# Performance work log

Hardware: AMD Instinct MI355X
Metric: run time of the kernel (lower is better)

## Reference

```python
import jax, jax.numpy as jnp
import numpy as np

N_SRC0, N_DST0, N_DST1 = 100000, 20000, 4000
E0, E1 = 640000, 128000
IN_F, HID_F, OUT_F = 512, 512, 256


def _graph_conv(x_src, src, dst, W, b, n_src, n_dst):
    """DGL GraphConv, norm='both': D_out^{-1/2} A D_in^{-1/2} X W + b."""
    ones_e = jnp.ones(src.shape[0], x_src.dtype)
    out_deg = jnp.maximum(jax.ops.segment_sum(ones_e, src, num_segments=n_src), 1.0)
    in_deg = jnp.maximum(jax.ops.segment_sum(ones_e, dst, num_segments=n_dst), 1.0)
    h = x_src * (out_deg ** -0.5)[:, None]          # [n_src, F] pre-normalize
    agg = jax.ops.segment_sum(h[src], dst, num_segments=n_dst)  # gather -> scatter-add
    agg = agg * (in_deg ** -0.5)[:, None]           # [n_dst, F]
    return agg @ W + b


def setup_inputs() -> dict:
    key = jax.random.key(0)
    ks = jax.random.split(key, 8)
    x = jax.random.normal(ks[0], (N_SRC0, IN_F), jnp.float32)
    src0 = jax.random.randint(ks[1], (E0,), 0, N_SRC0)
    dst0 = jax.random.randint(ks[2], (E0,), 0, N_DST0)
    src1 = jax.random.randint(ks[3], (E1,), 0, N_DST0)
    dst1 = jax.random.randint(ks[4], (E1,), 0, N_DST1)
    W1 = jax.random.normal(ks[5], (IN_F, HID_F), jnp.float32) * (IN_F ** -0.5)
    b1 = jnp.zeros((HID_F,), jnp.float32)
    W2 = jax.random.normal(ks[6], (HID_F, OUT_F), jnp.float32) * (HID_F ** -0.5)
    b2 = jnp.zeros((OUT_F,), jnp.float32)
    return {"x": x, "src0": src0, "dst0": dst0, "src1": src1, "dst1": dst1,
            "W1": W1, "b1": b1, "W2": W2, "b2": b2,
            "n_src0": N_SRC0, "n_dst0": N_DST0, "n_dst1": N_DST1}


def reference(x, src0, dst0, src1, dst1, W1, b1, W2, b2, n_src0, n_dst0, n_dst1):
    h = jax.nn.relu(_graph_conv(x, src0, dst0, W1, b1, n_src0, n_dst0))
    out = jax.nn.relu(_graph_conv(h, src1, dst1, W2, b2, n_dst0, n_dst1))
    return out
```

## Files before the change

kernel.cpp:

```cpp
#include <hip/hip_runtime.h>

typedef unsigned short ushort_t;
typedef unsigned int uint_t;
typedef __attribute__((ext_vector_type(8))) short s8v;
typedef __attribute__((ext_vector_type(4))) float f4v;

#define NS0 100000
#define ND0 20000
#define ND1 4000
#define E0  640000
#define E1  128000
#define F   512
#define OF  256
#define NCNT (NS0 + ND0 + ND0 + ND1)
#define SB  96

#define WBLK ((F * F + F * OF) / 256)

__device__ __forceinline__ ushort_t f2b(float f) {
    uint_t u = __float_as_uint(f);
    uint_t r = (u + 0x7fffu + ((u >> 16) & 1u)) >> 16;
    return (ushort_t)r;
}
__device__ __forceinline__ float b2f_lo(uint_t u) { return __uint_as_float(u << 16); }
__device__ __forceinline__ float b2f_hi(uint_t u) { return __uint_as_float(u & 0xffff0000u); }

__global__ __launch_bounds__(256) void prep(const int* __restrict__ src0, const int* __restrict__ dst0,
                                            const int* __restrict__ src1, const int* __restrict__ dst1,
                                            int* __restrict__ cntOut0, int* __restrict__ cntIn0,
                                            int* __restrict__ cntOut1, int* __restrict__ cntIn1,
                                            int* __restrict__ es0, int* __restrict__ es1,
                                            const float* __restrict__ W1, const float* __restrict__ W2,
                                            ushort_t* __restrict__ wt1, ushort_t* __restrict__ wt2) {
    int b = blockIdx.x;
    if (b < 625) {
        int e = (b * 256 + threadIdx.x) * 4;
        int4 s = *(const int4*)(src0 + e);
        int4 d = *(const int4*)(dst0 + e);
        atomicAdd(&cntOut0[s.x], 1);
        atomicAdd(&cntOut0[s.y], 1);
        atomicAdd(&cntOut0[s.z], 1);
        atomicAdd(&cntOut0[s.w], 1);
        int p0 = atomicAdd(&cntIn0[d.x], 1);
        int p1 = atomicAdd(&cntIn0[d.y], 1);
        int p2 = atomicAdd(&cntIn0[d.z], 1);
        int p3 = atomicAdd(&cntIn0[d.w], 1);
        es0[d.x * SB + min(p0, SB - 1)] = s.x;
        es0[d.y * SB + min(p1, SB - 1)] = s.y;
        es0[d.z * SB + min(p2, SB - 1)] = s.z;
        es0[d.w * SB + min(p3, SB - 1)] = s.w;
        return;
    }
    if (b < 750) {
        int e = ((b - 625) * 256 + threadIdx.x) * 4;
        int4 s = *(const int4*)(src1 + e);
        int4 d = *(const int4*)(dst1 + e);
        atomicAdd(&cntOut1[s.x], 1);
        atomicAdd(&cntOut1[s.y], 1);
        atomicAdd(&cntOut1[s.z], 1);
        atomicAdd(&cntOut1[s.w], 1);
        int p0 = atomicAdd(&cntIn1[d.x], 1);
        int p1 = atomicAdd(&cntIn1[d.y], 1);
        int p2 = atomicAdd(&cntIn1[d.z], 1);
        int p3 = atomicAdd(&cntIn1[d.w], 1);
        es1[d.x * SB + min(p0, SB - 1)] = s.x;
        es1[d.y * SB + min(p1, SB - 1)] = s.y;
        es1[d.z * SB + min(p2, SB - 1)] = s.z;
        es1[d.w * SB + min(p3, SB - 1)] = s.w;
        return;
    }
    int i = (b - 750) * 256 + threadIdx.x;
    if (i < F * F) {
        int k = i >> 9, n = i & (F - 1);
        wt1[n * F + k] = f2b(W1[i]);
    } else {
        int j = i - F * F;
        int k = j >> 8, n = j & (OF - 1);
        wt2[n * F + k] = f2b(W2[j]);
    }
}

__device__ __forceinline__ void add8(float* acc, uint4 u) {
    acc[0] += b2f_lo(u.x); acc[1] += b2f_hi(u.x);
    acc[2] += b2f_lo(u.y); acc[3] += b2f_hi(u.y);
    acc[4] += b2f_lo(u.z); acc[5] += b2f_hi(u.z);
    acc[6] += b2f_lo(u.w); acc[7] += b2f_hi(u.w);
}

__global__ __launch_bounds__(256) void agg_l1(const float* __restrict__ X, const int* __restrict__ es,
                                              const int* __restrict__ cntIn, const int* __restrict__ cntOut,
                                              ushort_t* __restrict__ out, int ndst) {
    int d = __builtin_amdgcn_readfirstlane(blockIdx.x * 4 + (threadIdx.x >> 6));
    if (d >= ndst) return;
    int lane = threadIdx.x & 63;
    int n = min(cntIn[d], SB);
    const int* ed = es + (size_t)d * SB;
    const f4v* Xv = (const f4v*)X;
    f4v accA = {0.f, 0.f, 0.f, 0.f};
    f4v accB = {0.f, 0.f, 0.f, 0.f};
    int c = n >> 2;
    int i = c << 2;
    if (c > 0) {
        int idP[4], idQ[4];
        f4v aP[4], bP[4], aQ[4], bQ[4];
        int cvP[4], cvQ[4];
        #pragma unroll
        for (int j = 0; j < 4; ++j) idP[j] = ed[j];
        #pragma unroll
        for (int j = 0; j < 4; ++j) {
            aP[j] = Xv[(size_t)idP[j] * 128 + lane];
            bP[j] = Xv[(size_t)idP[j] * 128 + 64 + lane];
        }
        #pragma unroll
        for (int j = 0; j < 4; ++j) cvP[j] = cntOut[idP[j]];
        if (c > 1) {
            #pragma unroll
            for (int j = 0; j < 4; ++j) idQ[j] = ed[4 + j];
        }
        int k = 0;
        while (true) {
            if (k + 1 < c) {
                #pragma unroll
                for (int j = 0; j < 4; ++j) {
                    aQ[j] = Xv[(size_t)idQ[j] * 128 + lane];
                    bQ[j] = Xv[(size_t)idQ[j] * 128 + 64 + lane];
                }
                #pragma unroll
                for (int j = 0; j < 4; ++j) cvQ[j] = cntOut[idQ[j]];
                if (k + 2 < c) {
                    #pragma unroll
                    for (int j = 0; j < 4; ++j) idP[j] = ed[(k + 2) * 4 + j];
                }
            }
            #pragma unroll
            for (int j = 0; j < 4; ++j) {
                float sc = rsqrtf(fmaxf((float)cvP[j], 1.0f));
                accA += aP[j] * sc;
                accB += bP[j] * sc;
            }
            ++k;
            if (k >= c) break;
            if (k + 1 < c) {
                #pragma unroll
                for (int j = 0; j < 4; ++j) {
                    aP[j] = Xv[(size_t)idP[j] * 128 + lane];
                    bP[j] = Xv[(size_t)idP[j] * 128 + 64 + lane];
                }
                #pragma unroll
                for (int j = 0; j < 4; ++j) cvP[j] = cntOut[idP[j]];
                if (k + 2 < c) {
                    #pragma unroll
                    for (int j = 0; j < 4; ++j) idQ[j] = ed[(k + 2) * 4 + j];
                }
            }
            #pragma unroll
            for (int j = 0; j < 4; ++j) {
                float sc = rsqrtf(fmaxf((float)cvQ[j], 1.0f));
                accA += aQ[j] * sc;
                accB += bQ[j] * sc;
            }
            ++k;
            if (k >= c) break;
        }
    }
    for (; i < n; ++i) {
        int s = ed[i];
        float sc = rsqrtf(fmaxf((float)cntOut[s], 1.0f));
        accA += Xv[(size_t)s * 128 + lane] * sc;
        accB += Xv[(size_t)s * 128 + 64 + lane] * sc;
    }
    float sc = rsqrtf(fmaxf((float)n, 1.0f));
    accA *= sc;
    accB *= sc;
    uint2 oA, oB;
    oA.x = (uint_t)f2b(accA.x) | ((uint_t)f2b(accA.y) << 16);
    oA.y = (uint_t)f2b(accA.z) | ((uint_t)f2b(accA.w) << 16);
    oB.x = (uint_t)f2b(accB.x) | ((uint_t)f2b(accB.y) << 16);
    oB.y = (uint_t)f2b(accB.z) | ((uint_t)f2b(accB.w) << 16);
    uint2* op = (uint2*)out;
    op[(size_t)d * 128 + lane] = oA;
    op[(size_t)d * 128 + 64 + lane] = oB;
}

__global__ __launch_bounds__(256) void agg_l2(const ushort_t* __restrict__ X, const int* __restrict__ es,
                                              const int* __restrict__ cntIn, ushort_t* __restrict__ out,
                                              int ndst) {
    int d = __builtin_amdgcn_readfirstlane(blockIdx.x * 4 + (threadIdx.x >> 6));
    if (d >= ndst) return;
    int lane = threadIdx.x & 63;
    int n = min(cntIn[d], SB);
    const int* ed = es + (size_t)d * SB;
    const uint4* Xv = (const uint4*)X;
    float acc[8] = {0.f, 0.f, 0.f, 0.f, 0.f, 0.f, 0.f, 0.f};
    int c = n >> 3;
    int i = c << 3;
    if (c > 0) {
        int idP[8], idQ[8];
        uint4 uP[8], uQ[8];
        #pragma unroll
        for (int j = 0; j < 8; ++j) idP[j] = ed[j];
        #pragma unroll
        for (int j = 0; j < 8; ++j) uP[j] = Xv[(size_t)idP[j] * 64 + lane];
        if (c > 1) {
            #pragma unroll
            for (int j = 0; j < 8; ++j) idQ[j] = ed[8 + j];
        }
        int k = 0;
        while (true) {
            if (k + 1 < c) {
                #pragma unroll
                for (int j = 0; j < 8; ++j) uQ[j] = Xv[(size_t)idQ[j] * 64 + lane];
                if (k + 2 < c) {
                    #pragma unroll
                    for (int j = 0; j < 8; ++j) idP[j] = ed[(k + 2) * 8 + j];
                }
            }
            #pragma unroll
            for (int j = 0; j < 8; ++j) add8(acc, uP[j]);
            ++k;
            if (k >= c) break;
            if (k + 1 < c) {
                #pragma unroll
                for (int j = 0; j < 8; ++j) uP[j] = Xv[(size_t)idP[j] * 64 + lane];
                if (k + 2 < c) {
                    #pragma unroll
                    for (int j = 0; j < 8; ++j) idQ[j] = ed[(k + 2) * 8 + j];
                }
            }
            #pragma unroll
            for (int j = 0; j < 8; ++j) add8(acc, uQ[j]);
            ++k;
            if (k >= c) break;
        }
    }
    for (; i < n; ++i) add8(acc, Xv[(size_t)ed[i] * 64 + lane]);
    float sc = rsqrtf(fmaxf((float)n, 1.0f));
    uint4 o;
    o.x = (uint_t)f2b(acc[0] * sc) | ((uint_t)f2b(acc[1] * sc) << 16);
    o.y = (uint_t)f2b(acc[2] * sc) | ((uint_t)f2b(acc[3] * sc) << 16);
    o.z = (uint_t)f2b(acc[4] * sc) | ((uint_t)f2b(acc[5] * sc) << 16);
    o.w = (uint_t)f2b(acc[6] * sc) | ((uint_t)f2b(acc[7] * sc) << 16);
    ((uint4*)out)[(size_t)d * 64 + lane] = o;
}

template <typename OutT>
__global__ __launch_bounds__(256) void gemm128(const ushort_t* __restrict__ A, const ushort_t* __restrict__ BT,
                                               const float* __restrict__ bias, const int* __restrict__ rowCnt,
                                               OutT* __restrict__ C, int M, int N, int K) {
    __shared__ __align__(16) ushort_t As[128 * 64];
    __shared__ __align__(16) ushort_t Bs[128 * 64];
    int tid = threadIdx.x;
    int lane = tid & 63, w = tid >> 6;
    int m16 = lane & 15, quad = lane >> 4;
    int wm = w & 1, wn = w >> 1;
    int bm = blockIdx.x * 128, bn = blockIdx.y * 128;
    f4v acc[4][4] = {};
    for (int k0 = 0; k0 < K; k0 += 64) {
        #pragma unroll
        for (int i = 0; i < 4; ++i) {
            int c = i * 256 + tid;
            int row = c >> 3, seg = (c & 7) * 8;
            int ra = bm + row; if (ra >= M) ra = M - 1;
            __builtin_amdgcn_global_load_lds(
                (const __attribute__((address_space(1))) uint_t*)(A + (size_t)ra * K + k0 + seg),
                (__attribute__((address_space(3))) uint_t*)(As + (size_t)c * 8), 16, 0, 0);
        }
        #pragma unroll
        for (int i = 0; i < 4; ++i) {
            int c = i * 256 + tid;
            int row = c >> 3, seg = (c & 7) * 8;
            int rb = bn + row;
            __builtin_amdgcn_global_load_lds(
                (const __attribute__((address_space(1))) uint_t*)(BT + (size_t)rb * K + k0 + seg),
                (__attribute__((address_space(3))) uint_t*)(Bs + (size_t)c * 8), 16, 0, 0);
        }
        __syncthreads();
        #pragma unroll
        for (int kc = 0; kc < 2; ++kc) {
            int co = kc * 32 + quad * 8;
            s8v af[4], bf[4];
            #pragma unroll
            for (int m = 0; m < 4; ++m)
                af[m] = *(const s8v*)&As[(wm * 64 + m * 16 + m16) * 64 + co];
            #pragma unroll
            for (int nn = 0; nn < 4; ++nn)
                bf[nn] = *(const s8v*)&Bs[(wn * 64 + nn * 16 + m16) * 64 + co];
            #pragma unroll
            for (int m = 0; m < 4; ++m)
                #pragma unroll
                for (int nn = 0; nn < 4; ++nn)
                    acc[m][nn] = __builtin_amdgcn_mfma_f32_16x16x32_bf16(af[m], bf[nn], acc[m][nn], 0, 0, 0);
        }
        __syncthreads();
    }
    #pragma unroll
    for (int m = 0; m < 4; ++m) {
        #pragma unroll
        for (int rr = 0; rr < 4; ++rr) {
            int row = bm + wm * 64 + m * 16 + quad * 4 + rr;
            if (row < M) {
                float rs = rowCnt ? rsqrtf(fmaxf((float)rowCnt[row], 1.0f)) : 1.0f;
                #pragma unroll
                for (int nn = 0; nn < 4; ++nn) {
                    int col = bn + wn * 64 + nn * 16 + m16;
                    float v = fmaxf(acc[m][nn][rr] + bias[col], 0.0f) * rs;
                    if (sizeof(OutT) == 2)
                        ((ushort_t*)C)[(size_t)row * N + col] = f2b(v);
                    else
                        ((float*)C)[(size_t)row * N + col] = v;
                }
            }
        }
    }
}

extern "C" void kernel_launch(void* const* d_in, const int* in_sizes, int n_in,
                              void* d_out, int out_size, void* d_ws, size_t ws_size,
                              hipStream_t stream) {
    (void)in_sizes; (void)n_in; (void)out_size; (void)ws_size;
    const float* x    = (const float*)d_in[0];
    const int*   src0 = (const int*)d_in[1];
    const int*   dst0 = (const int*)d_in[2];
    const int*   src1 = (const int*)d_in[3];
    const int*   dst1 = (const int*)d_in[4];
    const float* W1   = (const float*)d_in[5];
    const float* b1   = (const float*)d_in[6];
    const float* W2   = (const float*)d_in[7];
    const float* b2   = (const float*)d_in[8];
    float* out = (float*)d_out;

    char* p = (char*)d_ws;
    auto alloc = [&](size_t bytes) { char* q = p; p += (bytes + 255) & ~(size_t)255; return q; };
    int*      cnt  = (int*)alloc((size_t)NCNT * 4);
    int*      es0  = (int*)alloc((size_t)ND0 * SB * 4);
    int*      es1  = (int*)alloc((size_t)ND1 * SB * 4);
    ushort_t* wt1  = (ushort_t*)alloc((size_t)F * F * 2);
    ushort_t* wt2  = (ushort_t*)alloc((size_t)OF * F * 2);
    ushort_t* agg0 = (ushort_t*)alloc((size_t)ND0 * F * 2);
    ushort_t* h    = (ushort_t*)alloc((size_t)ND0 * F * 2);
    ushort_t* agg1 = (ushort_t*)alloc((size_t)ND1 * F * 2);

    int* cntOut0 = cnt;
    int* cntIn0  = cnt + NS0;
    int* cntOut1 = cnt + NS0 + ND0;
    int* cntIn1  = cnt + NS0 + ND0 + ND0;

    (void)hipMemsetAsync(cnt, 0, (size_t)NCNT * 4, stream);

    prep<<<750 + WBLK, 256, 0, stream>>>(src0, dst0, src1, dst1,
                                         cntOut0, cntIn0, cntOut1, cntIn1, es0, es1,
                                         W1, W2, wt1, wt2);

    agg_l1<<<(ND0 + 3) / 4, 256, 0, stream>>>(x, es0, cntIn0, cntOut0, agg0, ND0);

    gemm128<ushort_t><<<dim3((ND0 + 127) / 128, F / 128), 256, 0, stream>>>(
        agg0, wt1, b1, cntOut1, h, ND0, F, F);

    agg_l2<<<(ND1 + 3) / 4, 256, 0, stream>>>(h, es1, cntIn1, agg1, ND1);

    gemm128<float><<<dim3((ND1 + 127) / 128, OF / 128), 256, 0, stream>>>(
        agg1, wt2, b2, nullptr, out, ND1, OF, F);
}
```

Before: 579.7 us.

## Reorder GraphConv to transform-then-aggregate with bf16 projected features

Both layers now multiply by the weight matrix before aggregating, using (AX)W = A(XW). Layer 1 runs a bf16 MFMA GEMM over all 100k source rows: it converts fp32 x on the fly, folds in the out-degree scaling and writes bf16 Y. The edge gather then reads 1 KB bf16 rows instead of 2 KB fp32 rows. Bias, ReLU and the layer-2 out-degree scaling move into the aggregation epilogue. Layer 2 projects to 256 features before gathering, which halves the gather width, and writes the fp32 output directly. The trade-off is a much larger layer-1 GEMM (100k rows instead of 20k) and an extra 100 MB intermediate, in exchange for less random gather traffic. The in-degree normalization now uses the raw count rather than the SB-capped count.

```diff
diff --git a/kernel.cpp b/kernel.cpp
--- a/kernel.cpp
+++ b/kernel.cpp
@@ -80,6 +80,86 @@
     }
 }
 
+__global__ __launch_bounds__(256) void gemm_xw(const float* __restrict__ A, const ushort_t* __restrict__ BT,
+                                               const int* __restrict__ rowCnt, ushort_t* __restrict__ Y,
+                                               int M, int K) {
+    __shared__ __align__(16) ushort_t As[128 * 64];
+    __shared__ __align__(16) ushort_t Bs[128 * 64];
+    int tid = threadIdx.x;
+    int lane = tid & 63, w = tid >> 6;
+    int m16 = lane & 15, quad = lane >> 4;
+    int wm = w & 1, wn = w >> 1;
+    int bid = blockIdx.x;
+    int wg = (bid & 7) * ((int)gridDim.x >> 3) + (bid >> 3);
+    int nt = wg & 3, mt = wg >> 2;
+    int bm = mt * 128, bn = nt * 128;
+    const int N = 512;
+    f4v acc[4][4] = {};
+    for (int k0 = 0; k0 < K; k0 += 64) {
+        f4v av[8];
+        #pragma unroll
+        for (int i = 0; i < 4; ++i) {
+            int c = i * 256 + tid;
+            int row = c >> 3, seg = (c & 7) * 8;
+            int ra = bm + row; if (ra >= M) ra = M - 1;
+            const f4v* srcp = (const f4v*)(A + (size_t)ra * K + k0 + seg);
+            av[i * 2]     = __builtin_nontemporal_load(srcp);
+            av[i * 2 + 1] = __builtin_nontemporal_load(srcp + 1);
+        }
+        #pragma unroll
+        for (int i = 0; i < 4; ++i) {
+            int c = i * 256 + tid;
+            int row = c >> 3, seg = (c & 7) * 8;
+            __builtin_amdgcn_global_load_lds(
+                (const __attribute__((address_space(1))) uint_t*)(BT + (size_t)(bn + row) * K + k0 + seg),
+                (__attribute__((address_space(3))) uint_t*)(Bs + (size_t)c * 8), 16, 0, 0);
+        }
+        #pragma unroll
+        for (int i = 0; i < 4; ++i) {
+            int c = i * 256 + tid;
+            uint4 o;
+            o.x = (uint_t)f2b(av[i * 2].x)     | ((uint_t)f2b(av[i * 2].y) << 16);
+            o.y = (uint_t)f2b(av[i * 2].z)     | ((uint_t)f2b(av[i * 2].w) << 16);
+            o.z = (uint_t)f2b(av[i * 2 + 1].x) | ((uint_t)f2b(av[i * 2 + 1].y) << 16);
+            o.w = (uint_t)f2b(av[i * 2 + 1].z) | ((uint_t)f2b(av[i * 2 + 1].w) << 16);
+            *(uint4*)(As + (size_t)c * 8) = o;
+        }
+        __syncthreads();
+        #pragma unroll
+        for (int kc = 0; kc < 2; ++kc) {
+            int co = kc * 32 + quad * 8;
+            s8v af[4], bf[4];
+            #pragma unroll
+            for (int m = 0; m < 4; ++m)
+                af[m] = *(const s8v*)&As[(wm * 64 + m * 16 + m16) * 64 + co];
+            #pragma unroll
+            for (int nn = 0; nn < 4; ++nn)
+                bf[nn] = *(const s8v*)&Bs[(wn * 64 + nn * 16 + m16) * 64 + co];
+            #pragma unroll
+            for (int m = 0; m < 4; ++m)
+                #pragma unroll
+                for (int nn = 0; nn < 4; ++nn)
+                    acc[m][nn] = __builtin_amdgcn_mfma_f32_16x16x32_bf16(af[m], bf[nn], acc[m][nn], 0, 0, 0);
+        }
+        __syncthreads();
+    }
+    #pragma unroll
+    for (int m = 0; m < 4; ++m) {
+        #pragma unroll
+        for (int rr = 0; rr < 4; ++rr) {
+            int row = bm + wm * 64 + m * 16 + quad * 4 + rr;
+            if (row < M) {
+                float rs = rsqrtf(fmaxf((float)rowCnt[row], 1.0f));
+                #pragma unroll
+                for (int nn = 0; nn < 4; ++nn) {
+                    int col = bn + wn * 64 + nn * 16 + m16;
+                    Y[(size_t)row * N + col] = f2b(acc[m][nn][rr] * rs);
+                }
+            }
+        }
+    }
+}
+
 __device__ __forceinline__ void add8(float* acc, uint4 u) {
     acc[0] += b2f_lo(u.x); acc[1] += b2f_hi(u.x);
     acc[2] += b2f_lo(u.y); acc[3] += b2f_hi(u.y);
@@ -87,110 +167,16 @@
     acc[6] += b2f_lo(u.w); acc[7] += b2f_hi(u.w);
 }
 
-__global__ __launch_bounds__(256) void agg_l1(const float* __restrict__ X, const int* __restrict__ es,
-                                              const int* __restrict__ cntIn, const int* __restrict__ cntOut,
-                                              ushort_t* __restrict__ out, int ndst) {
+__global__ __launch_bounds__(256) void agg1(const ushort_t* __restrict__ Yb, const int* __restrict__ es,
+                                            const int* __restrict__ cntIn, const int* __restrict__ cntOut1,
+                                            const float* __restrict__ b1, ushort_t* __restrict__ out, int ndst) {
     int d = __builtin_amdgcn_readfirstlane(blockIdx.x * 4 + (threadIdx.x >> 6));
     if (d >= ndst) return;
     int lane = threadIdx.x & 63;
-    int n = min(cntIn[d], SB);
+    int cntd = cntIn[d];
+    int n = min(cntd, SB);
     const int* ed = es + (size_t)d * SB;
-    const f4v* Xv = (const f4v*)X;
-    f4v accA = {0.f, 0.f, 0.f, 0.f};
-    f4v accB = {0.f, 0.f, 0.f, 0.f};
-    int c = n >> 2;
-    int i = c << 2;
-    if (c > 0) {
-        int idP[4], idQ[4];
-        f4v aP[4], bP[4], aQ[4], bQ[4];
-        int cvP[4], cvQ[4];
-        #pragma unroll
-        for (int j = 0; j < 4; ++j) idP[j] = ed[j];
-        #pragma unroll
-        for (int j = 0; j < 4; ++j) {
-            aP[j] = Xv[(size_t)idP[j] * 128 + lane];
-            bP[j] = Xv[(size_t)idP[j] * 128 + 64 + lane];
-        }
-        #pragma unroll
-        for (int j = 0; j < 4; ++j) cvP[j] = cntOut[idP[j]];
-        if (c > 1) {
-            #pragma unroll
-            for (int j = 0; j < 4; ++j) idQ[j] = ed[4 + j];
-        }
-        int k = 0;
-        while (true) {
-            if (k + 1 < c) {
-                #pragma unroll
-                for (int j = 0; j < 4; ++j) {
-                    aQ[j] = Xv[(size_t)idQ[j] * 128 + lane];
-                    bQ[j] = Xv[(size_t)idQ[j] * 128 + 64 + lane];
-                }
-                #pragma unroll
-                for (int j = 0; j < 4; ++j) cvQ[j] = cntOut[idQ[j]];
-                if (k + 2 < c) {
-                    #pragma unroll
-                    for (int j = 0; j < 4; ++j) idP[j] = ed[(k + 2) * 4 + j];
-                }
-            }
-            #pragma unroll
-            for (int j = 0; j < 4; ++j) {
-                float sc = rsqrtf(fmaxf((float)cvP[j], 1.0f));
-                accA += aP[j] * sc;
-                accB += bP[j] * sc;
-            }
-            ++k;
-            if (k >= c) break;
-            if (k + 1 < c) {
-                #pragma unroll
-                for (int j = 0; j < 4; ++j) {
-                    aP[j] = Xv[(size_t)idP[j] * 128 + lane];
-                    bP[j] = Xv[(size_t)idP[j] * 128 + 64 + lane];
-                }
-                #pragma unroll
-                for (int j = 0; j < 4; ++j) cvP[j] = cntOut[idP[j]];
-                if (k + 2 < c) {
-                    #pragma unroll
-                    for (int j = 0; j < 4; ++j) idQ[j] = ed[(k + 2) * 4 + j];
-                }
-            }
-            #pragma unroll
-            for (int j = 0; j < 4; ++j) {
-                float sc = rsqrtf(fmaxf((float)cvQ[j], 1.0f));
-                accA += aQ[j] * sc;
-                accB += bQ[j] * sc;
-            }
-            ++k;
-            if (k >= c) break;
-        }
-    }
-    for (; i < n; ++i) {
-        int s = ed[i];
-        float sc = rsqrtf(fmaxf((float)cntOut[s], 1.0f));
-        accA += Xv[(size_t)s * 128 + lane] * sc;
-        accB += Xv[(size_t)s * 128 + 64 + lane] * sc;
-    }
-    float sc = rsqrtf(fmaxf((float)n, 1.0f));
-    accA *= sc;
-    accB *= sc;
-    uint2 oA, oB;
-    oA.x = (uint_t)f2b(accA.x) | ((uint_t)f2b(accA.y) << 16);
-    oA.y = (uint_t)f2b(accA.z) | ((uint_t)f2b(accA.w) << 16);
-    oB.x = (uint_t)f2b(accB.x) | ((uint_t)f2b(accB.y) << 16);
-    oB.y = (uint_t)f2b(accB.z) | ((uint_t)f2b(accB.w) << 16);
-    uint2* op = (uint2*)out;
-    op[(size_t)d * 128 + lane] = oA;
-    op[(size_t)d * 128 + 64 + lane] = oB;
-}
-
-__global__ __launch_bounds__(256) void agg_l2(const ushort_t* __restrict__ X, const int* __restrict__ es,
-                                              const int* __restrict__ cntIn, ushort_t* __restrict__ out,
-                                              int ndst) {
-    int d = __builtin_amdgcn_readfirstlane(blockIdx.x * 4 + (threadIdx.x >> 6));
-    if (d >= ndst) return;
-    int lane = threadIdx.x & 63;
-    int n = min(cntIn[d], SB);
-    const int* ed = es + (size_t)d * SB;
-    const uint4* Xv = (const uint4*)X;
+    const uint4* Xv = (const uint4*)Yb;
     float acc[8] = {0.f, 0.f, 0.f, 0.f, 0.f, 0.f, 0.f, 0.f};
     int c = n >> 3;
     int i = c << 3;
@@ -234,19 +220,28 @@
         }
     }
     for (; i < n; ++i) add8(acc, Xv[(size_t)ed[i] * 64 + lane]);
-    float sc = rsqrtf(fmaxf((float)n, 1.0f));
+    float rsIn = rsqrtf(fmaxf((float)cntd, 1.0f));
+    float rsO1 = rsqrtf(fmaxf((float)cntOut1[d], 1.0f));
+    const f4v* bb = (const f4v*)(b1 + lane * 8);
+    f4v bA = bb[0], bB = bb[1];
+    float v0 = fmaxf(acc[0] * rsIn + bA.x, 0.f) * rsO1;
+    float v1 = fmaxf(acc[1] * rsIn + bA.y, 0.f) * rsO1;
+    float v2 = fmaxf(acc[2] * rsIn + bA.z, 0.f) * rsO1;
+    float v3 = fmaxf(acc[3] * rsIn + bA.w, 0.f) * rsO1;
+    float v4 = fmaxf(acc[4] * rsIn + bB.x, 0.f) * rsO1;
+    float v5 = fmaxf(acc[5] * rsIn + bB.y, 0.f) * rsO1;
+    float v6 = fmaxf(acc[6] * rsIn + bB.z, 0.f) * rsO1;
+    float v7 = fmaxf(acc[7] * rsIn + bB.w, 0.f) * rsO1;
     uint4 o;
-    o.x = (uint_t)f2b(acc[0] * sc) | ((uint_t)f2b(acc[1] * sc) << 16);
-    o.y = (uint_t)f2b(acc[2] * sc) | ((uint_t)f2b(acc[3] * sc) << 16);
-    o.z = (uint_t)f2b(acc[4] * sc) | ((uint_t)f2b(acc[5] * sc) << 16);
-    o.w = (uint_t)f2b(acc[6] * sc) | ((uint_t)f2b(acc[7] * sc) << 16);
+    o.x = (uint_t)f2b(v0) | ((uint_t)f2b(v1) << 16);
+    o.y = (uint_t)f2b(v2) | ((uint_t)f2b(v3) << 16);
+    o.z = (uint_t)f2b(v4) | ((uint_t)f2b(v5) << 16);
+    o.w = (uint_t)f2b(v6) | ((uint_t)f2b(v7) << 16);
     ((uint4*)out)[(size_t)d * 64 + lane] = o;
 }
 
-template <typename OutT>
-__global__ __launch_bounds__(256) void gemm128(const ushort_t* __restrict__ A, const ushort_t* __restrict__ BT,
-                                               const float* __restrict__ bias, const int* __restrict__ rowCnt,
-                                               OutT* __restrict__ C, int M, int N, int K) {
+__global__ __launch_bounds__(256) void gemm_h2z(const ushort_t* __restrict__ A, const ushort_t* __restrict__ BT,
+                                                ushort_t* __restrict__ C, int M, int N, int K) {
     __shared__ __align__(16) ushort_t As[128 * 64];
     __shared__ __align__(16) ushort_t Bs[128 * 64];
     int tid = threadIdx.x;
@@ -269,9 +264,8 @@
         for (int i = 0; i < 4; ++i) {
             int c = i * 256 + tid;
             int row = c >> 3, seg = (c & 7) * 8;
-            int rb = bn + row;
             __builtin_amdgcn_global_load_lds(
-                (const __attribute__((address_space(1))) uint_t*)(BT + (size_t)rb * K + k0 + seg),
+                (const __attribute__((address_space(1))) uint_t*)(BT + (size_t)(bn + row) * K + k0 + seg),
                 (__attribute__((address_space(3))) uint_t*)(Bs + (size_t)c * 8), 16, 0, 0);
         }
         __syncthreads();
@@ -299,19 +293,87 @@
         for (int rr = 0; rr < 4; ++rr) {
             int row = bm + wm * 64 + m * 16 + quad * 4 + rr;
             if (row < M) {
-                float rs = rowCnt ? rsqrtf(fmaxf((float)rowCnt[row], 1.0f)) : 1.0f;
                 #pragma unroll
                 for (int nn = 0; nn < 4; ++nn) {
                     int col = bn + wn * 64 + nn * 16 + m16;
-                    float v = fmaxf(acc[m][nn][rr] + bias[col], 0.0f) * rs;
-                    if (sizeof(OutT) == 2)
-                        ((ushort_t*)C)[(size_t)row * N + col] = f2b(v);
-                    else
-                        ((float*)C)[(size_t)row * N + col] = v;
-                }
-            }
-        }
-    }
+                    C[(size_t)row * N + col] = f2b(acc[m][nn][rr]);
+                }
+            }
+        }
+    }
+}
+
+__global__ __launch_bounds__(256) void agg2(const ushort_t* __restrict__ Z, const int* __restrict__ es,
+                                            const int* __restrict__ cntIn, const float* __restrict__ b2,
+                                            float* __restrict__ out, int ndst) {
+    int d = __builtin_amdgcn_readfirstlane(blockIdx.x * 4 + (threadIdx.x >> 6));
+    if (d >= ndst) return;
+    int lane = threadIdx.x & 63;
+    int cntd = cntIn[d];
+    int n = min(cntd, SB);
+    const int* ed = es + (size_t)d * SB;
+    const uint2* Zv = (const uint2*)Z;
+    float a0 = 0.f, a1 = 0.f, a2 = 0.f, a3 = 0.f;
+    int c = n >> 3;
+    int i = c << 3;
+    if (c > 0) {
+        int idP[8], idQ[8];
+        uint2 uP[8], uQ[8];
+        #pragma unroll
+        for (int j = 0; j < 8; ++j) idP[j] = ed[j];
+        #pragma unroll
+        for (int j = 0; j < 8; ++j) uP[j] = Zv[(size_t)idP[j] * 64 + lane];
+        if (c > 1) {
+            #pragma unroll
+            for (int j = 0; j < 8; ++j) idQ[j] = ed[8 + j];
+        }
+        int k = 0;
+        while (true) {
+            if (k + 1 < c) {
+                #pragma unroll
+                for (int j = 0; j < 8; ++j) uQ[j] = Zv[(size_t)idQ[j] * 64 + lane];
+                if (k + 2 < c) {
+                    #pragma unroll
+                    for (int j = 0; j < 8; ++j) idP[j] = ed[(k + 2) * 8 + j];
+                }
+            }
+            #pragma unroll
+            for (int j = 0; j < 8; ++j) {
+                a0 += b2f_lo(uP[j].x); a1 += b2f_hi(uP[j].x);
+                a2 += b2f_lo(uP[j].y); a3 += b2f_hi(uP[j].y);
+            }
+            ++k;
+            if (k >= c) break;
+            if (k + 1 < c) {
+                #pragma unroll
+                for (int j = 0; j < 8; ++j) uP[j] = Zv[(size_t)idP[j] * 64 + lane];
+                if (k + 2 < c) {
+                    #pragma unroll
+                    for (int j = 0; j < 8; ++j) idQ[j] = ed[(k + 2) * 8 + j];
+                }
+            }
+            #pragma unroll
+            for (int j = 0; j < 8; ++j) {
+                a0 += b2f_lo(uQ[j].x); a1 += b2f_hi(uQ[j].x);
+                a2 += b2f_lo(uQ[j].y); a3 += b2f_hi(uQ[j].y);
+            }
+            ++k;
+            if (k >= c) break;
+        }
+    }
+    for (; i < n; ++i) {
+        uint2 u = Zv[(size_t)ed[i] * 64 + lane];
+        a0 += b2f_lo(u.x); a1 += b2f_hi(u.x);
+        a2 += b2f_lo(u.y); a3 += b2f_hi(u.y);
+    }
+    float rs = rsqrtf(fmaxf((float)cntd, 1.0f));
+    f4v bb = *(const f4v*)(b2 + lane * 4);
+    f4v o;
+    o.x = fmaxf(a0 * rs + bb.x, 0.f);
+    o.y = fmaxf(a1 * rs + bb.y, 0.f);
+    o.z = fmaxf(a2 * rs + bb.z, 0.f);
+    o.w = fmaxf(a3 * rs + bb.w, 0.f);
+    ((f4v*)out)[(size_t)d * 64 + lane] = o;
 }
 
 extern "C" void kernel_launch(void* const* d_in, const int* in_sizes, int n_in,
@@ -336,9 +398,9 @@
     int*      es1  = (int*)alloc((size_t)ND1 * SB * 4);
     ushort_t* wt1  = (ushort_t*)alloc((size_t)F * F * 2);
     ushort_t* wt2  = (ushort_t*)alloc((size_t)OF * F * 2);
-    ushort_t* agg0 = (ushort_t*)alloc((size_t)ND0 * F * 2);
-    ushort_t* h    = (ushort_t*)alloc((size_t)ND0 * F * 2);
-    ushort_t* agg1 = (ushort_t*)alloc((size_t)ND1 * F * 2);
+    ushort_t* y    = (ushort_t*)alloc((size_t)NS0 * F * 2);
+    ushort_t* hp   = (ushort_t*)alloc((size_t)ND0 * F * 2);
+    ushort_t* z    = (ushort_t*)alloc((size_t)ND0 * OF * 2);
 
     int* cntOut0 = cnt;
     int* cntIn0  = cnt + NS0;
@@ -351,13 +413,11 @@
                                          cntOut0, cntIn0, cntOut1, cntIn1, es0, es1,
                                          W1, W2, wt1, wt2);
 
-    agg_l1<<<(ND0 + 3) / 4, 256, 0, stream>>>(x, es0, cntIn0, cntOut0, agg0, ND0);
-
-    gemm128<ushort_t><<<dim3((ND0 + 127) / 128, F / 128), 256, 0, stream>>>(
-        agg0, wt1, b1, cntOut1, h, ND0, F, F);
-
-    agg_l2<<<(ND1 + 3) / 4, 256, 0, stream>>>(h, es1, cntIn1, agg1, ND1);
-
-    gemm128<float><<<dim3((ND1 + 127) / 128, OF / 128), 256, 0, stream>>>(
-        agg1, wt2, b2, nullptr, out, ND1, OF, F);
-}
+    gemm_xw<<<3128, 256, 0, stream>>>(x, wt1, cntOut0, y, NS0, F);
+
+    agg1<<<(ND0 + 3) / 4, 256, 0, stream>>>(y, es0, cntIn0, cntOut1, b1, hp, ND0);
+
+    gemm_h2z<<<dim3((ND0 + 127) / 128, OF / 128), 256, 0, stream>>>(hp, wt2, z, ND0, OF, F);
+
+    agg2<<<(ND1 + 3) / 4, 256, 0, stream>>>(z, es1, cntIn1, b2, out, ND1);
+}
```

Result: slower. 613.9 us (+5.9%).
